# Performance work log

Hardware: AMD Instinct MI355X
Metric: run time of the kernel (lower is better)

The kernel has to match this reference:

```python
import jax, jax.numpy as jnp
import numpy as np

TMSG = 15  # max_len - 1


def setup_inputs() -> dict:
    key = jax.random.key(0)
    ks = jax.random.split(key, 8)
    B, T_in, E, H, V = 4096, 4, 256, 512, 32000
    s = lambda k, shape: jax.random.normal(k, shape, jnp.float32) * 0.05
    return {
        "inp": jax.random.normal(ks[0], (B, T_in, E), jnp.float32),
        "Wx0": s(ks[1], (E, 4 * H)),
        "Wh0": s(ks[2], (H, 4 * H)),
        "b0": jnp.zeros((4 * H,), jnp.float32),
        "Wx1": s(ks[3], (H, 4 * H)),
        "Wh1": s(ks[4], (H, 4 * H)),
        "b1": jnp.zeros((4 * H,), jnp.float32),
        "Wd": s(ks[5], (H, V)),
        "bd": jnp.zeros((V,), jnp.float32),
    }


def _lstm_step(x, h, c, Wx, Wh, b):
    # Keras LSTMCell gate order: i, f, g(cell), o
    z = x @ Wx + h @ Wh + b
    i, f, g, o = jnp.split(z, 4, axis=-1)
    c = jax.nn.sigmoid(f) * c + jax.nn.sigmoid(i) * jnp.tanh(g)
    h = jax.nn.sigmoid(o) * jnp.tanh(c)
    return h, c


def reference(inp, Wx0, Wh0, b0, Wx1, Wh1, b1, Wd, bd):
    B = inp.shape[0]
    H = Wh0.shape[0]
    z = jnp.zeros((B, H), inp.dtype)

    def scan_fn(carry, x_t):
        h0, c0, h1, c1 = carry
        h0, c0 = _lstm_step(x_t, h0, c0, Wx0, Wh0, b0)
        h1, c1 = _lstm_step(h0, h1, c1, Wx1, Wh1, b1)
        return (h0, c0, h1, c1), None

    # NOTE: source bug resets initial_state to None every step, so each of the
    # max_len-1 steps runs the identical stacked LSTM from zero state; we run it once.
    (h0, c0, h1, c1), _ = jax.lax.scan(scan_fn, (z, z, z, z), jnp.swapaxes(inp, 0, 1))
    out = h1  # (B, H) last-step output of top cell

    log_probs = jax.nn.log_softmax(out @ Wd + bd, axis=-1)  # (B, V)
    probs = jnp.exp(log_probs)
    entropy = -jnp.sum(probs * log_probs, axis=-1)  # (B,)

    keys = jax.random.split(jax.random.key(42), TMSG)
    samples = jax.vmap(lambda k: jax.random.categorical(k, log_probs, axis=-1))(keys)  # (T, B)
    lp = log_probs[jnp.arange(B)[None, :], samples]  # (T, B) log_prob of sampled chars
    ent = jnp.broadcast_to(entropy[None], (TMSG, B))  # (T, B)

    message = samples.T  # (B, T)
    message = jnp.concatenate([message, jnp.zeros_like(message)], axis=1)  # (B, 2T)
    state_h = jnp.stack([h0, c0])  # keras unpack quirk: states[0] = [h, c] of cell 0
    return (message, lp, ent, state_h)
```

## Files before the change

kernel.cpp:

```cpp
#include <hip/hip_runtime.h>
#include <stdint.h>
#include <math.h>

#define BB 4096
#define HH 512
#define VV 32000
#define NT 15
#define STF 2097152

struct KeysArg { uint32_t w[2*NT]; };

__host__ __device__ inline void tf2x32(uint32_t k0, uint32_t k1,
                                       uint32_t x0, uint32_t x1,
                                       uint32_t& o0, uint32_t& o1) {
  uint32_t ks2 = k0 ^ k1 ^ 0x1BD11BDAu;
  x0 += k0; x1 += k1;
#define TF_R(r) { x0 += x1; x1 = (x1 << (r)) | (x1 >> (32 - (r))); x1 ^= x0; }
  TF_R(13) TF_R(15) TF_R(26) TF_R(6)
  x0 += k1; x1 += ks2 + 1u;
  TF_R(17) TF_R(29) TF_R(16) TF_R(24)
  x0 += ks2; x1 += k0 + 2u;
  TF_R(13) TF_R(15) TF_R(26) TF_R(6)
  x0 += k0; x1 += k1 + 3u;
  TF_R(17) TF_R(29) TF_R(16) TF_R(24)
  x0 += k1; x1 += ks2 + 4u;
  TF_R(13) TF_R(15) TF_R(26) TF_R(6)
  x0 += ks2; x1 += k0 + 5u;
#undef TF_R
  o0 = x0; o1 = x1;
}

__global__ __launch_bounds__(256)
void gemm_sk(const float* __restrict__ A0, int lda0,
             const float* __restrict__ W0, int koff0, int Klen0,
             const float* __restrict__ A1, int lda1,
             const float* __restrict__ W1, int koff1, int Klen1,
             int ldw,
             const float* __restrict__ bias,
             float* __restrict__ C0, float* __restrict__ C1, int ldc)
{
  const float* A; const float* W; float* C; int lda, koff, Klen;
  if (blockIdx.z == 0) { A = A0; lda = lda0; W = W0; koff = koff0; Klen = Klen0; C = C0; }
  else                 { A = A1; lda = lda1; W = W1; koff = koff1; Klen = Klen1; C = C1; }

  __shared__ float As[2][16][128];
  __shared__ float Ws[2][16][128];
  const int tid = threadIdx.x;
  const int m0 = blockIdx.y * 128;
  const int n0 = blockIdx.x * 128;
  const int tx = tid & 15, ty = tid >> 4;
  float acc[8][8];
  #pragma unroll
  for (int i = 0; i < 8; ++i)
    #pragma unroll
    for (int j = 0; j < 8; ++j) acc[i][j] = 0.0f;

  const int sr = tid >> 1, sc = (tid & 1) * 8;
  const int wk = tid >> 4, wn = (tid & 15) * 4;

  float4 av0, av1, wv0, wv1;
  auto LOAD = [&](int kt) {
    const int k0 = koff + (kt << 4);
    const float* asrc = A + (size_t)(m0 + sr) * lda + (k0 + sc);
    av0 = *(const float4*)asrc;
    av1 = *(const float4*)(asrc + 4);
    const float* wsrc = W + (size_t)(k0 + wk) * ldw + (n0 + wn);
    wv0 = *(const float4*)wsrc;
    wv1 = *(const float4*)(wsrc + 64);
  };
  auto STORE = [&](int buf) {
    As[buf][sc+0][sr]=av0.x; As[buf][sc+1][sr]=av0.y;
    As[buf][sc+2][sr]=av0.z; As[buf][sc+3][sr]=av0.w;
    As[buf][sc+4][sr]=av1.x; As[buf][sc+5][sr]=av1.y;
    As[buf][sc+6][sr]=av1.z; As[buf][sc+7][sr]=av1.w;
    *(float4*)&Ws[buf][wk][wn]      = wv0;
    *(float4*)&Ws[buf][wk][wn + 64] = wv1;
  };

  const int nkt = Klen >> 4;
  if (nkt > 0) { LOAD(0); STORE(0); }
  __syncthreads();

  int cur = 0;
  for (int kt = 0; kt < nkt; ++kt) {
    const bool more = (kt + 1 < nkt);
    if (more) LOAD(kt + 1);
    #pragma unroll
    for (int kk = 0; kk < 16; ++kk) {
      float4 a0 = *(const float4*)&As[cur][kk][ty*8];
      float4 a1 = *(const float4*)&As[cur][kk][ty*8+4];
      float4 b0 = *(const float4*)&Ws[cur][kk][tx*4];
      float4 b1 = *(const float4*)&Ws[cur][kk][tx*4+64];
      float ar[8] = {a0.x,a0.y,a0.z,a0.w,a1.x,a1.y,a1.z,a1.w};
      float br[8] = {b0.x,b0.y,b0.z,b0.w,b1.x,b1.y,b1.z,b1.w};
      #pragma unroll
      for (int i = 0; i < 8; ++i)
        #pragma unroll
        for (int j = 0; j < 8; ++j)
          acc[i][j] = fmaf(ar[i], br[j], acc[i][j]);
    }
    if (more) STORE(cur ^ 1);
    __syncthreads();
    cur ^= 1;
  }

  #pragma unroll
  for (int i = 0; i < 8; ++i) {
    const int m = m0 + ty*8 + i;
    float* dst = C + (size_t)m * ldc + (n0 + wn);
    float4 o0, o1;
    o0.x = acc[i][0]; o0.y = acc[i][1]; o0.z = acc[i][2]; o0.w = acc[i][3];
    o1.x = acc[i][4]; o1.y = acc[i][5]; o1.z = acc[i][6]; o1.w = acc[i][7];
    if (bias) {
      o0.x += bias[n0+wn+0]; o0.y += bias[n0+wn+1];
      o0.z += bias[n0+wn+2]; o0.w += bias[n0+wn+3];
      o1.x += bias[n0+wn+64]; o1.y += bias[n0+wn+65];
      o1.z += bias[n0+wn+66]; o1.w += bias[n0+wn+67];
    }
    *(float4*)dst        = o0;
    *(float4*)(dst + 64) = o1;
  }
}

__global__ __launch_bounds__(256)
void gate_kernel(const float* __restrict__ z0, const float* __restrict__ z1,
                 const float* __restrict__ bias,
                 const float* __restrict__ cin,
                 float* __restrict__ hout, float* __restrict__ cout,
                 float* __restrict__ sh, float* __restrict__ sc)
{
  int idx = blockIdx.x * 256 + threadIdx.x;
  int b = idx >> 9, j = idx & 511;
  const size_t r2 = (size_t)b * 2048;
  float zi = z0[r2+j]      + z1[r2+j]      + bias[j];
  float zf = z0[r2+j+512]  + z1[r2+j+512]  + bias[j+512];
  float zg = z0[r2+j+1024] + z1[r2+j+1024] + bias[j+1024];
  float zo = z0[r2+j+1536] + z1[r2+j+1536] + bias[j+1536];
  float si = 1.0f/(1.0f+expf(-zi));
  float sf = 1.0f/(1.0f+expf(-zf));
  float so = 1.0f/(1.0f+expf(-zo));
  float c = sf * cin[idx] + si * tanhf(zg);
  float h = so * tanhf(c);
  cout[idx] = c; hout[idx] = h;
  if (sh) { sh[idx] = h; sc[idx] = c; }
}

__global__ __launch_bounds__(256)
void rowstat_kernel(const float* __restrict__ logits,
                    float* __restrict__ rowM, float* __restrict__ rowLS,
                    float* __restrict__ rowEnt)
{
  const int row = blockIdx.x;
  const float* x = logits + (size_t)row * VV;
  const int tid = threadIdx.x;
  float m = -INFINITY;
  for (int v = tid; v < VV; v += 256) m = fmaxf(m, x[v]);
  #pragma unroll
  for (int off = 32; off; off >>= 1) m = fmaxf(m, __shfl_down(m, off));
  __shared__ float sm[4], ssum[4], swsum[4];
  if ((tid & 63) == 0) sm[tid >> 6] = m;
  __syncthreads();
  m = fmaxf(fmaxf(sm[0], sm[1]), fmaxf(sm[2], sm[3]));
  float s = 0.0f, w = 0.0f;
  for (int v = tid; v < VV; v += 256) {
    float d = x[v] - m;
    float e = expf(d);
    s += e; w += d * e;
  }
  #pragma unroll
  for (int off = 32; off; off >>= 1) { s += __shfl_down(s, off); w += __shfl_down(w, off); }
  if ((tid & 63) == 0) { ssum[tid >> 6] = s; swsum[tid >> 6] = w; }
  __syncthreads();
  if (tid == 0) {
    s = ssum[0]+ssum[1]+ssum[2]+ssum[3];
    w = swsum[0]+swsum[1]+swsum[2]+swsum[3];
    float ls = logf(s);
    rowM[row] = m; rowLS[row] = ls; rowEnt[row] = ls - w / s;
  }
}

__global__ __launch_bounds__(256)
void sample_kernel(const float* __restrict__ logits,
                   const float* __restrict__ rowM, const float* __restrict__ rowLS,
                   const float* __restrict__ rowEnt,
                   float* __restrict__ out,
                   KeysArg keys, int bbase)
{
  const int l = blockIdx.x;
  const int b = bbase + l;
  const float* x = logits + (size_t)l * VV;
  const float m = rowM[l], ls = rowLS[l];

  float bv[NT];
  uint32_t bi[NT];
  float thr[NT];
  #pragma unroll
  for (int t = 0; t < NT; ++t) { bv[t] = -INFINITY; bi[t] = 0; thr[t] = 1.0f; }

  const uint32_t pbase = (uint32_t)b * (uint32_t)VV;
  for (int v = threadIdx.x; v < VV; v += 256) {
    const float lp = (x[v] - m) - ls;
    const uint32_t p = pbase + (uint32_t)v;
    #pragma unroll
    for (int t = 0; t < NT; ++t) {
      uint32_t o0, o1;
      tf2x32(keys.w[2*t], keys.w[2*t+1], 0u, p, o0, o1);
      const uint32_t bits = o0 ^ o1;
      const float uf = __uint_as_float((bits >> 9) | 0x3f800000u);
      if (__any(uf >= thr[t])) {
        float u = fmaxf(uf - 1.0f, 1.17549435e-38f);
        float g = -logf(-logf(u)) + lp;
        bool improved = (uf >= thr[t]) && (g > bv[t]);
        if (improved) { bv[t] = g; bi[t] = (uint32_t)v; }
        if (__any(improved)) {
          float wb = bv[t];
          #pragma unroll
          for (int off = 1; off < 64; off <<= 1)
            wb = fmaxf(wb, __shfl_xor(wb, off));
          float us = expf(-expf(-(wb + ls)));
          thr[t] = 1.0f + us * 0.999999f;
        }
      }
    }
  }

  __shared__ float rv[NT][4];
  __shared__ uint32_t ri[NT][4];
  const int lane = threadIdx.x & 63, wq = threadIdx.x >> 6;
  #pragma unroll
  for (int t = 0; t < NT; ++t) {
    float v = bv[t]; uint32_t idx = bi[t];
    #pragma unroll
    for (int off = 32; off; off >>= 1) {
      float ov = __shfl_down(v, off);
      uint32_t oi = __shfl_down(idx, off);
      if (ov > v || (ov == v && oi < idx)) { v = ov; idx = oi; }
    }
    if (lane == 0) { rv[t][wq] = v; ri[t][wq] = idx; }
  }
  __syncthreads();
  if (threadIdx.x < NT) {
    const int t = threadIdx.x;
    float v = rv[t][0]; uint32_t idx = ri[t][0];
    #pragma unroll
    for (int q = 1; q < 4; ++q) {
      float ov = rv[t][q]; uint32_t oi = ri[t][q];
      if (ov > v || (ov == v && oi < idx)) { v = ov; idx = oi; }
    }
    out[(size_t)b * 30 + t]      = (float)idx;
    out[(size_t)b * 30 + 15 + t] = 0.0f;
    out[122880 + (size_t)t * BB + b] = (x[idx] - m) - ls;
    out[184320 + (size_t)t * BB + b] = rowEnt[l];
  }
}

extern "C" void kernel_launch(void* const* d_in, const int* in_sizes, int n_in,
                              void* d_out, int out_size, void* d_ws, size_t ws_size,
                              hipStream_t stream)
{
  const float* inp = (const float*)d_in[0];
  const float* Wx0 = (const float*)d_in[1];
  const float* Wh0 = (const float*)d_in[2];
  const float* b0v = (const float*)d_in[3];
  const float* Wx1 = (const float*)d_in[4];
  const float* Wh1 = (const float*)d_in[5];
  const float* b1v = (const float*)d_in[6];
  const float* Wd  = (const float*)d_in[7];
  const float* bdv = (const float*)d_in[8];
  float* out = (float*)d_out;
  float* ws = (float*)d_ws;

  float* h0 = ws;
  float* c0 = ws + (size_t)STF;
  float* h1 = ws + (size_t)2*STF;
  float* c1 = ws + (size_t)3*STF;
  float* rowM  = ws + (size_t)4*STF;
  float* rowLS = rowM + 4096;
  float* rowEnt = rowLS + 4096;
  float* region = ws + (size_t)4*STF + 12288;
  float* z0 = region;
  float* z1 = region + (size_t)4096*2048;
  float* logits = region;

  size_t ws_floats = ws_size / 4;
  size_t base = (size_t)4*STF + 12288;
  int CH = 4096;
  while (CH > 128 && base + (size_t)CH*VV > ws_floats) CH >>= 1;

  hipMemsetAsync(ws, 0, (size_t)4*STF*sizeof(float), stream);

  for (int t = 0; t < 4; ++t) {
    gemm_sk<<<dim3(2048/128, 4096/128, 2), 256, 0, stream>>>(
        h0, 512, Wh0, 0, 512,
        inp + t*256, 1024, Wx0, 0, 256,
        2048, nullptr, z0, z1, 2048);
    gate_kernel<<<STF/256, 256, 0, stream>>>(
        z0, z1, b0v, c0, h0, c0,
        (t==3) ? out + 245760 : (float*)nullptr,
        (t==3) ? out + 245760 + STF : (float*)nullptr);
    gemm_sk<<<dim3(2048/128, 4096/128, 2), 256, 0, stream>>>(
        h0, 512, Wx1, 0, 512,
        h1, 512, Wh1, 0, 512,
        2048, nullptr, z0, z1, 2048);
    gate_kernel<<<STF/256, 256, 0, stream>>>(
        z0, z1, b1v, c1, h1, c1, (float*)nullptr, (float*)nullptr);
  }

  KeysArg ka;
  for (int t = 0; t < NT; ++t) {
    uint32_t o0, o1;
    tf2x32(0u, 42u, 0u, (uint32_t)t, o0, o1);
    ka.w[2*t] = o0; ka.w[2*t+1] = o1;
  }

  const int nch = 4096 / CH;
  for (int c = 0; c < nch; ++c) {
    int bbase = c * CH;
    gemm_sk<<<dim3(VV/128, CH/128, 1), 256, 0, stream>>>(
        h1 + (size_t)bbase*512, 512, Wd, 0, 512,
        nullptr, 0, nullptr, 0, 0,
        VV, bdv, logits, nullptr, VV);
    rowstat_kernel<<<CH, 256, 0, stream>>>(logits, rowM, rowLS, rowEnt);
    sample_kernel<<<CH, 256, 0, stream>>>(logits, rowM, rowLS, rowEnt, out, ka, bbase);
  }
}
```

Measured before the change: 8.194 ms.

## Stage GEMM tiles directly into LDS via global_load_lds with row-major A layout

Replaces the register-staged global-to-shared copies in the fp32 GEMM with direct global-to-LDS async loads, so A is stored row-major (no transpose scatter) and W is copied as-is. The inner loop is restructured to read eight A float4s per four k-steps and reuse them across the W reads. The intent is to cut register pressure and VALU/LDS-store instructions for staging and to overlap the next tile's loads with compute. The risk is that row-major A reads (stride 16 floats across ty) cause LDS bank conflicts, and the vmcnt(0) wait serializes at the end of each step. It also drops the nkt>0 guard on the first stage.

```diff
diff --git a/kernel.cpp b/kernel.cpp
--- a/kernel.cpp
+++ b/kernel.cpp
@@ -30,6 +30,12 @@
   o0 = x0; o1 = x1;
 }
 
+__device__ inline void gll16(const float* g, float* l) {
+  __builtin_amdgcn_global_load_lds(
+      (const __attribute__((address_space(1))) void*)g,
+      (__attribute__((address_space(3))) void*)l, 16, 0, 0);
+}
+
 __global__ __launch_bounds__(256)
 void gemm_sk(const float* __restrict__ A0, int lda0,
              const float* __restrict__ W0, int koff0, int Klen0,
@@ -43,70 +49,78 @@
   if (blockIdx.z == 0) { A = A0; lda = lda0; W = W0; koff = koff0; Klen = Klen0; C = C0; }
   else                 { A = A1; lda = lda1; W = W1; koff = koff1; Klen = Klen1; C = C1; }
 
-  __shared__ float As[2][16][128];
-  __shared__ float Ws[2][16][128];
+  __shared__ float As[2][128 * 16];
+  __shared__ float Ws[2][16 * 128];
   const int tid = threadIdx.x;
+  const int lane = tid & 63, wv = tid >> 6;
   const int m0 = blockIdx.y * 128;
   const int n0 = blockIdx.x * 128;
   const int tx = tid & 15, ty = tid >> 4;
+
   float acc[8][8];
   #pragma unroll
   for (int i = 0; i < 8; ++i)
     #pragma unroll
     for (int j = 0; j < 8; ++j) acc[i][j] = 0.0f;
 
-  const int sr = tid >> 1, sc = (tid & 1) * 8;
-  const int wk = tid >> 4, wn = (tid & 15) * 4;
-
-  float4 av0, av1, wv0, wv1;
-  auto LOAD = [&](int kt) {
+  const int a_row_in = (lane >> 2);
+  const int a_chunk  = (lane & 3) * 4;
+  const int w_row_in = (lane >> 5);
+  const int w_col    = (lane & 31) * 4;
+
+  auto STAGE = [&](int buf, int kt) {
     const int k0 = koff + (kt << 4);
-    const float* asrc = A + (size_t)(m0 + sr) * lda + (k0 + sc);
-    av0 = *(const float4*)asrc;
-    av1 = *(const float4*)(asrc + 4);
-    const float* wsrc = W + (size_t)(k0 + wk) * ldw + (n0 + wn);
-    wv0 = *(const float4*)wsrc;
-    wv1 = *(const float4*)(wsrc + 64);
+    #pragma unroll
+    for (int i = 0; i < 2; ++i) {
+      const int seg = wv * 2 + i;
+      const int arow = seg * 16 + a_row_in;
+      gll16(A + (size_t)(m0 + arow) * lda + (k0 + a_chunk),
+            &As[buf][seg * 256]);
+      const int wrow = seg * 2 + w_row_in;
+      gll16(W + (size_t)(k0 + wrow) * ldw + (n0 + w_col),
+            &Ws[buf][seg * 256]);
+    }
   };
-  auto STORE = [&](int buf) {
-    As[buf][sc+0][sr]=av0.x; As[buf][sc+1][sr]=av0.y;
-    As[buf][sc+2][sr]=av0.z; As[buf][sc+3][sr]=av0.w;
-    As[buf][sc+4][sr]=av1.x; As[buf][sc+5][sr]=av1.y;
-    As[buf][sc+6][sr]=av1.z; As[buf][sc+7][sr]=av1.w;
-    *(float4*)&Ws[buf][wk][wn]      = wv0;
-    *(float4*)&Ws[buf][wk][wn + 64] = wv1;
-  };
 
   const int nkt = Klen >> 4;
-  if (nkt > 0) { LOAD(0); STORE(0); }
+  STAGE(0, 0);
+  asm volatile("s_waitcnt vmcnt(0)" ::: "memory");
   __syncthreads();
 
   int cur = 0;
   for (int kt = 0; kt < nkt; ++kt) {
-    const bool more = (kt + 1 < nkt);
-    if (more) LOAD(kt + 1);
-    #pragma unroll
-    for (int kk = 0; kk < 16; ++kk) {
-      float4 a0 = *(const float4*)&As[cur][kk][ty*8];
-      float4 a1 = *(const float4*)&As[cur][kk][ty*8+4];
-      float4 b0 = *(const float4*)&Ws[cur][kk][tx*4];
-      float4 b1 = *(const float4*)&Ws[cur][kk][tx*4+64];
-      float ar[8] = {a0.x,a0.y,a0.z,a0.w,a1.x,a1.y,a1.z,a1.w};
-      float br[8] = {b0.x,b0.y,b0.z,b0.w,b1.x,b1.y,b1.z,b1.w};
+    if (kt + 1 < nkt) STAGE(cur ^ 1, kt + 1);
+    #pragma unroll
+    for (int kk4 = 0; kk4 < 4; ++kk4) {
+      float4 a4[8];
       #pragma unroll
-      for (int i = 0; i < 8; ++i)
+      for (int mm = 0; mm < 8; ++mm)
+        a4[mm] = *(const float4*)&As[cur][(ty * 8 + mm) * 16 + kk4 * 4];
+      #pragma unroll
+      for (int q = 0; q < 4; ++q) {
+        const int kk = kk4 * 4 + q;
+        float4 b0 = *(const float4*)&Ws[cur][kk * 128 + tx * 4];
+        float4 b1 = *(const float4*)&Ws[cur][kk * 128 + tx * 4 + 64];
+        float br[8] = {b0.x,b0.y,b0.z,b0.w,b1.x,b1.y,b1.z,b1.w};
         #pragma unroll
-        for (int j = 0; j < 8; ++j)
-          acc[i][j] = fmaf(ar[i], br[j], acc[i][j]);
-    }
-    if (more) STORE(cur ^ 1);
+        for (int mm = 0; mm < 8; ++mm) {
+          float av = (q == 0) ? a4[mm].x : (q == 1) ? a4[mm].y
+                   : (q == 2) ? a4[mm].z : a4[mm].w;
+          #pragma unroll
+          for (int j = 0; j < 8; ++j)
+            acc[mm][j] = fmaf(av, br[j], acc[mm][j]);
+        }
+      }
+    }
+    asm volatile("s_waitcnt vmcnt(0)" ::: "memory");
     __syncthreads();
     cur ^= 1;
   }
 
+  const int wn = tx * 4;
   #pragma unroll
   for (int i = 0; i < 8; ++i) {
-    const int m = m0 + ty*8 + i;
+    const int m = m0 + ty * 8 + i;
     float* dst = C + (size_t)m * ldc + (n0 + wn);
     float4 o0, o1;
     o0.x = acc[i][0]; o0.y = acc[i][1]; o0.z = acc[i][2]; o0.w = acc[i][3];
```

Result: faster. 7.285 ms (-11.1%).
